# Optimization experiments

Hardware: AMD Instinct MI355X
Metric: run time of the kernel (lower is better)

## Reference

```python
import jax, jax.numpy as jnp
import numpy as np

C, C_H, N_HEAD = 8, 1, 8
B, S, I = 1, 4096, 1024


def setup_inputs() -> dict:
    key = jax.random.key(0)
    ks = jax.random.split(key, 8)
    m = jax.random.normal(ks[0], (B, S, I, C), dtype=jnp.float32)
    mask = jnp.ones((B, S, I), dtype=jnp.float32)
    sc = 0.1
    return {
        "m": m,
        "mask": mask,
        "ln_gamma": jnp.ones((C,), jnp.float32),
        "ln_beta": jnp.zeros((C,), jnp.float32),
        "Wq": jax.random.normal(ks[1], (C, C_H * N_HEAD), jnp.float32) * sc,
        "Wk": jax.random.normal(ks[2], (C, C_H), jnp.float32) * sc,
        "Wv": jax.random.normal(ks[3], (C, C_H), jnp.float32) * sc,
        "Wg": jax.random.normal(ks[4], (C, C_H * N_HEAD), jnp.float32) * sc,
        "bg": jax.random.normal(ks[5], (C_H * N_HEAD,), jnp.float32) * sc,
        "Wo": jax.random.normal(ks[6], (C_H * N_HEAD, C), jnp.float32) * sc,
        "bo": jax.random.normal(ks[7], (C,), jnp.float32) * sc,
    }


def reference(m, mask, ln_gamma, ln_beta, Wq, Wk, Wv, Wg, bg, Wo, bo):
    # m: (B, s, i, c) -> work in (B, i, s, c); mask: (B, s, i) -> (B, i, s)
    mt = jnp.swapaxes(m, -2, -3)
    mk = jnp.swapaxes(mask, -1, -2)
    c_h = Wk.shape[1]
    h = Wq.shape[1] // c_h
    Bz, iz, sz, _ = mt.shape

    # LayerNorm over channel dim (eps=1e-5, population variance)
    mu = jnp.mean(mt, axis=-1, keepdims=True)
    var = jnp.mean(jnp.square(mt - mu), axis=-1, keepdims=True)
    mn = (mt - mu) / jnp.sqrt(var + 1e-5) * ln_gamma + ln_beta  # (B,i,s,c)

    # Masked mean pool over sequences -> global query per residue column
    q = jnp.sum(mn * mk[..., None], axis=-2) / (jnp.sum(mk, axis=-1)[..., None] + 1e-5)  # (B,i,c)

    q = (q @ Wq) * (c_h ** -0.5)          # (B,i,h*c_h)
    k = mn @ Wk                           # (B,i,s,c_h)  shared across heads
    v = mn @ Wv                           # (B,i,s,c_h)
    g = jax.nn.sigmoid(mn @ Wg + bg)      # (B,i,s,h*c_h)

    q = q.reshape(Bz, iz, h, c_h)
    g = g.reshape(Bz, iz, sz, h, c_h)

    bias = 1e9 * (mk - 1.0)               # (B,i,s)
    a = jnp.einsum('bihd,bisd->bihs', q, k) + bias[..., None, :]
    a = jax.nn.softmax(a, axis=-1)        # (B,i,h,s)
    o = jnp.einsum('bihs,bisd->bihd', a, v)  # (B,i,h,c_h)

    o = o[..., None, :, :] * g            # (B,i,s,h,c_h) gated, broadcast over s
    o = o.reshape(Bz, iz, sz, h * c_h) @ Wo + bo  # (B,i,s,c)
    return jnp.swapaxes(o, -2, -3)        # (B,s,i,c)
```

## Files before the change

### kernel.cpp

```cpp
#include <hip/hip_runtime.h>

#define I_LEN 1024

__device__ __forceinline__ float bf2f(unsigned int lo16) {
  unsigned int u = lo16 << 16;
  float f; __builtin_memcpy(&f, &u, 4); return f;
}
__device__ __forceinline__ unsigned int f2bf(float f) {
  unsigned int u; __builtin_memcpy(&u, &f, 4);
  return (u + 0x7FFFu + ((u >> 16) & 1u)) >> 16;
}

__global__ __launch_bounds__(1024) void msa_k1(
    const float* __restrict__ m, const float* __restrict__ mask,
    const float* __restrict__ lng, const float* __restrict__ lnb,
    const float* __restrict__ Wq, const float* __restrict__ Wk,
    const float* __restrict__ Wv, float* __restrict__ o_tab)
{
  __shared__ unsigned int kvs[4096 * 4];
  __shared__ float red[16][4][16];
  __shared__ float fin[4][9];
  __shared__ float qtab[4][8];

  const int t    = threadIdx.x;
  const int col  = t & 3;
  const int r    = t >> 2;
  const int lane = t & 63;
  const int wave = t >> 6;
  const int icol = blockIdx.x * 4 + col;

  float swk = 0.f, swv = 0.f, kb = 0.f, vb = 0.f;
#pragma unroll
  for (int c = 0; c < 8; ++c) {
    swk = fmaf(lng[c], Wk[c], swk);  swv = fmaf(lng[c], Wv[c], swv);
    kb  = fmaf(lnb[c], Wk[c], kb);   vb  = fmaf(lnb[c], Wv[c], vb);
  }

  unsigned int mb = 0;
  float qnx[8] = {0,0,0,0,0,0,0,0};
  float qd = 0.0f;

#pragma unroll 2
  for (int j = 0; j < 16; ++j) {
    const int s = r + 256 * j;
    const float4* mp = (const float4*)(m + (size_t)(s * I_LEN + icol) * 8);
    float4 lo = mp[0], hi = mp[1];
    const float mk = mask[s * I_LEN + icol];
    float x[8] = {lo.x, lo.y, lo.z, lo.w, hi.x, hi.y, hi.z, hi.w};
    float su = 0.f, s2 = 0.f;
#pragma unroll
    for (int c = 0; c < 8; ++c) { su += x[c]; s2 = fmaf(x[c], x[c], s2); }
    const float mu   = su * 0.125f;
    const float var  = s2 * 0.125f - mu * mu;
    const float rstd = rsqrtf(var + 1e-5f);
    float dk = 0.f, dv = 0.f;
#pragma unroll
    for (int c = 0; c < 8; ++c) {
      const float xg = x[c] * lng[c];
      dk = fmaf(xg, Wk[c], dk);
      dv = fmaf(xg, Wv[c], dv);
      x[c] = xg;
    }
    const float kk  = fmaf(rstd, fmaf(-mu, swk, dk), kb);
    const float vv  = fmaf(rstd, fmaf(-mu, swv, dv), vb);
    const float mr  = mk * rstd;
    const float mmr = -mu * mr;
#pragma unroll
    for (int c = 0; c < 8; ++c)
      qnx[c] = fmaf(x[c], mr, fmaf(lng[c], mmr, qnx[c]));
    qd += mk;
    kvs[s * 4 + col] = (f2bf(kk) << 16) | f2bf(vv);
    mb |= (mk > 0.5f ? 1u : 0u) << j;
  }

#pragma unroll
  for (int q = 0; q < 9; ++q) {
    float x = (q < 8) ? qnx[q] : qd;
#pragma unroll
    for (int off = 4; off <= 32; off <<= 1) x += __shfl_xor(x, off, 64);
    if (lane < 4) red[wave][lane][q] = x;
  }
  __syncthreads();
  if (t < 36) {
    int cc = t / 9, q = t - cc * 9;
    float s = 0.f;
#pragma unroll
    for (int w = 0; w < 16; ++w) s += red[w][cc][q];
    fin[cc][q] = s;
  }
  __syncthreads();
  if (t < 32) {
    int cc = t >> 3, h = t & 7;
    const float invd = 1.0f / (fin[cc][8] + 1e-5f);
    float qv = 0.f;
#pragma unroll
    for (int c = 0; c < 8; ++c) {
      const float qn = fmaf(lnb[c], fin[cc][8], fin[cc][c]);
      qv = fmaf(qn * invd, Wq[c * 8 + h], qv);
    }
    qtab[cc][h] = qv;
  }
  __syncthreads();

  float qh[8];
#pragma unroll
  for (int h = 0; h < 8; ++h) qh[h] = qtab[col][h];

  float se[8] = {0,0,0,0,0,0,0,0};
  float sv[8] = {0,0,0,0,0,0,0,0};
#pragma unroll 4
  for (int j = 0; j < 16; ++j) {
    const unsigned int w = kvs[(r + 256 * j) * 4 + col];
    const float kk = bf2f(w >> 16);
    const float vv = bf2f(w & 0xFFFFu);
    const float on = ((mb >> j) & 1u) ? 1.0f : 0.0f;
#pragma unroll
    for (int h = 0; h < 8; ++h) {
      const float e = __expf(qh[h] * kk) * on;
      se[h] += e;
      sv[h] = fmaf(e, vv, sv[h]);
    }
  }
#pragma unroll
  for (int q = 0; q < 16; ++q) {
    float x = (q < 8) ? se[q] : sv[q - 8];
#pragma unroll
    for (int off = 4; off <= 32; off <<= 1) x += __shfl_xor(x, off, 64);
    if (lane < 4) red[wave][lane][q] = x;
  }
  __syncthreads();
  if (t < 32) {
    int cc = t >> 3, h = t & 7;
    float a = 0.f, b = 0.f;
#pragma unroll
    for (int w = 0; w < 16; ++w) { a += red[w][cc][h]; b += red[w][cc][8 + h]; }
    o_tab[(blockIdx.x * 4 + cc) * 8 + h] = b / a;
  }
}

__global__ __launch_bounds__(256, 2) void msa_k2(
    const float* __restrict__ m,
    const float* __restrict__ lng, const float* __restrict__ lnb,
    const float* __restrict__ Wg, const float* __restrict__ bg,
    const float* __restrict__ Wo, const float* __restrict__ bo,
    const float* __restrict__ o_tab, float* __restrict__ out)
{
  const int tid = blockIdx.x * 256 + threadIdx.x;
  const int i = tid & (I_LEN - 1);

  float sgv[8], tbv[8];
#pragma unroll
  for (int h = 0; h < 8; ++h) {
    float s = 0.f, tb = bg[h];
#pragma unroll
    for (int c = 0; c < 8; ++c) {
      s  = fmaf(lng[c], Wg[c * 8 + h], s);
      tb = fmaf(lnb[c], Wg[c * 8 + h], tb);
    }
    sgv[h] = s; tbv[h] = tb;
  }

  const float4* op = (const float4*)(o_tab + i * 8);
  const float4 o1 = op[0], o2 = op[1];
  const float A[8] = {o1.x, o1.y, o1.z, o1.w, o2.x, o2.y, o2.z, o2.w};

#pragma unroll 2
  for (int q = 0; q < 8; ++q) {
    const size_t p = (size_t)tid + (size_t)q * 524288;
    const float4* mp = (const float4*)(m + p * 8);
    const float4 lo = mp[0], hi = mp[1];
    float x[8] = {lo.x, lo.y, lo.z, lo.w, hi.x, hi.y, hi.z, hi.w};
    float su = 0.f, s2 = 0.f;
#pragma unroll
    for (int c = 0; c < 8; ++c) { su += x[c]; s2 = fmaf(x[c], x[c], s2); }
    const float mu   = su * 0.125f;
    const float var  = s2 * 0.125f - mu * mu;
    const float rstd = rsqrtf(var + 1e-5f);
#pragma unroll
    for (int c = 0; c < 8; ++c) x[c] *= lng[c];
    float acc[8];
#pragma unroll
    for (int c = 0; c < 8; ++c) acc[c] = bo[c];
#pragma unroll
    for (int h = 0; h < 8; ++h) {
      float d = 0.f;
#pragma unroll
      for (int c = 0; c < 8; ++c) d = fmaf(x[c], Wg[c * 8 + h], d);
      const float gl = fmaf(rstd, fmaf(-mu, sgv[h], d), tbv[h]);
      const float gv = A[h] / (1.0f + __expf(-gl));
#pragma unroll
      for (int c = 0; c < 8; ++c) acc[c] = fmaf(gv, Wo[h * 8 + c], acc[c]);
    }
    float4* outp = (float4*)(out + p * 8);
    outp[0] = make_float4(acc[0], acc[1], acc[2], acc[3]);
    outp[1] = make_float4(acc[4], acc[5], acc[6], acc[7]);
  }
}

extern "C" void kernel_launch(void* const* d_in, const int* in_sizes, int n_in,
                              void* d_out, int out_size, void* d_ws, size_t ws_size,
                              hipStream_t stream) {
  const float* m    = (const float*)d_in[0];
  const float* mask = (const float*)d_in[1];
  const float* lng  = (const float*)d_in[2];
  const float* lnb  = (const float*)d_in[3];
  const float* Wq   = (const float*)d_in[4];
  const float* Wk   = (const float*)d_in[5];
  const float* Wv   = (const float*)d_in[6];
  const float* Wg   = (const float*)d_in[7];
  const float* bg   = (const float*)d_in[8];
  const float* Wo   = (const float*)d_in[9];
  const float* bo   = (const float*)d_in[10];
  float* out   = (float*)d_out;
  float* o_tab = (float*)d_ws;

  hipLaunchKernelGGL(msa_k1, dim3(256), dim3(1024), 0, stream,
                     m, mask, lng, lnb, Wq, Wk, Wv, o_tab);
  hipLaunchKernelGGL(msa_k2, dim3(2048), dim3(256), 0, stream,
                     m, lng, lnb, Wg, bg, Wo, bo, o_tab, out);
}
```

Baseline: 307.9 us.

## Split attention pass into parallel partial-reduction kernels and precompute quantized gates

Replaces the single low-parallelism column-reduction kernel with four kernels. A 2048-block LayerNorm pass computes K/V (packed as fp16, with a sentinel value for masked rows) and the sigmoid gates, stored as 16-bit fixed point. Small kernels then reduce the per-block partial sums for the pooled query and for the softmax numerator and denominator. The output kernel no longer rereads m or recomputes LayerNorm: it reads the packed gates and writes with nontemporal stores. This trades extra intermediate memory traffic and launches for much higher occupancy, and it lowers gate and K/V precision.

Result: slower. 331.0 us (+7.5%).

```diff
diff --git a/kernel.cpp b/kernel.cpp
--- a/kernel.cpp
+++ b/kernel.cpp
@@ -1,199 +1,312 @@
 #include <hip/hip_runtime.h>
 
 #define I_LEN 1024
-
-__device__ __forceinline__ float bf2f(unsigned int lo16) {
-  unsigned int u = lo16 << 16;
-  float f; __builtin_memcpy(&f, &u, 4); return f;
-}
-__device__ __forceinline__ unsigned int f2bf(float f) {
-  unsigned int u; __builtin_memcpy(&u, &f, 4);
-  return (u + 0x7FFFu + ((u >> 16) & 1u)) >> 16;
-}
-
-__global__ __launch_bounds__(1024) void msa_k1(
+#define S_LEN 4096
+
+typedef float f32x4 __attribute__((ext_vector_type(4)));
+
+__device__ __forceinline__ unsigned int f2h(float f) {
+  _Float16 h = (_Float16)f; unsigned short u;
+  __builtin_memcpy(&u, &h, 2); return (unsigned int)u;
+}
+__device__ __forceinline__ float h2f(unsigned int u) {
+  unsigned short s = (unsigned short)u; _Float16 h;
+  __builtin_memcpy(&h, &s, 2); return (float)h;
+}
+
+__global__ __launch_bounds__(256, 2) void msa_k1a(
     const float* __restrict__ m, const float* __restrict__ mask,
     const float* __restrict__ lng, const float* __restrict__ lnb,
-    const float* __restrict__ Wq, const float* __restrict__ Wk,
-    const float* __restrict__ Wv, float* __restrict__ o_tab)
-{
-  __shared__ unsigned int kvs[4096 * 4];
-  __shared__ float red[16][4][16];
-  __shared__ float fin[4][9];
-  __shared__ float qtab[4][8];
-
-  const int t    = threadIdx.x;
-  const int col  = t & 3;
-  const int r    = t >> 2;
-  const int lane = t & 63;
-  const int wave = t >> 6;
-  const int icol = blockIdx.x * 4 + col;
+    const float* __restrict__ Wk, const float* __restrict__ Wv,
+    const float* __restrict__ Wg, const float* __restrict__ bg,
+    unsigned int* __restrict__ kvS, uint4* __restrict__ glS,
+    float* __restrict__ qpart)
+{
+  const int b  = blockIdx.x;
+  const int cg = b & 15;
+  const int sb = b >> 4;
+  const int t  = threadIdx.x;
+  const int w  = t >> 6;
+  const int l  = t & 63;
+  const int i  = cg * 64 + w * 16 + (l & 15);
+  const int sg = l >> 4;
+  const int s0 = sb * 32 + sg * 8;
 
   float swk = 0.f, swv = 0.f, kb = 0.f, vb = 0.f;
+  float sgv[8], tbv[8];
 #pragma unroll
   for (int c = 0; c < 8; ++c) {
     swk = fmaf(lng[c], Wk[c], swk);  swv = fmaf(lng[c], Wv[c], swv);
     kb  = fmaf(lnb[c], Wk[c], kb);   vb  = fmaf(lnb[c], Wv[c], vb);
   }
-
-  unsigned int mb = 0;
+#pragma unroll
+  for (int h = 0; h < 8; ++h) {
+    float sv_ = 0.f, tb = bg[h];
+#pragma unroll
+    for (int c = 0; c < 8; ++c) {
+      sv_ = fmaf(lng[c], Wg[c * 8 + h], sv_);
+      tb  = fmaf(lnb[c], Wg[c * 8 + h], tb);
+    }
+    sgv[h] = sv_; tbv[h] = tb;
+  }
+
   float qnx[8] = {0,0,0,0,0,0,0,0};
-  float qd = 0.0f;
-
-#pragma unroll 2
-  for (int j = 0; j < 16; ++j) {
-    const int s = r + 256 * j;
-    const float4* mp = (const float4*)(m + (size_t)(s * I_LEN + icol) * 8);
-    float4 lo = mp[0], hi = mp[1];
-    const float mk = mask[s * I_LEN + icol];
-    float x[8] = {lo.x, lo.y, lo.z, lo.w, hi.x, hi.y, hi.z, hi.w};
-    float su = 0.f, s2 = 0.f;
-#pragma unroll
-    for (int c = 0; c < 8; ++c) { su += x[c]; s2 = fmaf(x[c], x[c], s2); }
-    const float mu   = su * 0.125f;
-    const float var  = s2 * 0.125f - mu * mu;
-    const float rstd = rsqrtf(var + 1e-5f);
-    float dk = 0.f, dv = 0.f;
-#pragma unroll
-    for (int c = 0; c < 8; ++c) {
-      const float xg = x[c] * lng[c];
-      dk = fmaf(xg, Wk[c], dk);
-      dv = fmaf(xg, Wv[c], dv);
-      x[c] = xg;
-    }
-    const float kk  = fmaf(rstd, fmaf(-mu, swk, dk), kb);
-    const float vv  = fmaf(rstd, fmaf(-mu, swv, dv), vb);
-    const float mr  = mk * rstd;
-    const float mmr = -mu * mr;
-#pragma unroll
-    for (int c = 0; c < 8; ++c)
-      qnx[c] = fmaf(x[c], mr, fmaf(lng[c], mmr, qnx[c]));
-    qd += mk;
-    kvs[s * 4 + col] = (f2bf(kk) << 16) | f2bf(vv);
-    mb |= (mk > 0.5f ? 1u : 0u) << j;
-  }
-
+  float qd = 0.f;
+
+#pragma unroll
+  for (int half = 0; half < 2; ++half) {
+    float4 L[4], H[4]; float MK[4];
+#pragma unroll
+    for (int r = 0; r < 4; ++r) {
+      const int s = s0 + half * 4 + r;
+      const size_t base = (size_t)(s * I_LEN + i);
+      const float4* mp = (const float4*)(m + base * 8);
+      L[r] = mp[0]; H[r] = mp[1];
+      MK[r] = mask[base];
+    }
+#pragma unroll
+    for (int r = 0; r < 4; ++r) {
+      const int s = s0 + half * 4 + r;
+      const size_t base = (size_t)(s * I_LEN + i);
+      float x[8] = {L[r].x, L[r].y, L[r].z, L[r].w, H[r].x, H[r].y, H[r].z, H[r].w};
+      const float mk = MK[r];
+      float su = 0.f, s2 = 0.f;
+#pragma unroll
+      for (int c = 0; c < 8; ++c) { su += x[c]; s2 = fmaf(x[c], x[c], s2); }
+      const float mu   = su * 0.125f;
+      const float var  = s2 * 0.125f - mu * mu;
+      const float rstd = rsqrtf(var + 1e-5f);
+      float dk = 0.f, dv = 0.f;
+#pragma unroll
+      for (int c = 0; c < 8; ++c) {
+        const float xg = x[c] * lng[c];
+        dk = fmaf(xg, Wk[c], dk);
+        dv = fmaf(xg, Wv[c], dv);
+        x[c] = xg;
+      }
+      const float kk = fmaf(rstd, fmaf(-mu, swk, dk), kb);
+      const float vv = fmaf(rstd, fmaf(-mu, swv, dv), vb);
+
+      unsigned int gw[4];
+#pragma unroll
+      for (int j = 0; j < 4; ++j) {
+        float d0 = 0.f, d1 = 0.f;
+#pragma unroll
+        for (int c = 0; c < 8; ++c) {
+          d0 = fmaf(x[c], Wg[c * 8 + 2 * j],     d0);
+          d1 = fmaf(x[c], Wg[c * 8 + 2 * j + 1], d1);
+        }
+        const float gl0 = fmaf(rstd, fmaf(-mu, sgv[2 * j],     d0), tbv[2 * j]);
+        const float gl1 = fmaf(rstd, fmaf(-mu, sgv[2 * j + 1], d1), tbv[2 * j + 1]);
+        const float g0 = 65535.f / (1.0f + __expf(-gl0));
+        const float g1 = 65535.f / (1.0f + __expf(-gl1));
+        const unsigned int u0 = (unsigned int)__float2int_rn(g0);
+        const unsigned int u1 = (unsigned int)__float2int_rn(g1);
+        gw[j] = u0 | (u1 << 16);
+      }
+      glS[base] = make_uint4(gw[0], gw[1], gw[2], gw[3]);
+      kvS[base] = (mk > 0.5f) ? ((f2h(kk) << 16) | f2h(vv)) : 0xFFFFFFFFu;
+
+      const float mr  = mk * rstd;
+      const float mmr = -mu * mr;
+#pragma unroll
+      for (int c = 0; c < 8; ++c)
+        qnx[c] = fmaf(x[c], mr, fmaf(lng[c], mmr, qnx[c]));
+      qd += mk;
+    }
+  }
+
+  float red[9];
 #pragma unroll
   for (int q = 0; q < 9; ++q) {
     float x = (q < 8) ? qnx[q] : qd;
-#pragma unroll
-    for (int off = 4; off <= 32; off <<= 1) x += __shfl_xor(x, off, 64);
-    if (lane < 4) red[wave][lane][q] = x;
-  }
-  __syncthreads();
-  if (t < 36) {
-    int cc = t / 9, q = t - cc * 9;
-    float s = 0.f;
-#pragma unroll
-    for (int w = 0; w < 16; ++w) s += red[w][cc][q];
-    fin[cc][q] = s;
-  }
-  __syncthreads();
-  if (t < 32) {
-    int cc = t >> 3, h = t & 7;
-    const float invd = 1.0f / (fin[cc][8] + 1e-5f);
-    float qv = 0.f;
-#pragma unroll
-    for (int c = 0; c < 8; ++c) {
-      const float qn = fmaf(lnb[c], fin[cc][8], fin[cc][c]);
-      qv = fmaf(qn * invd, Wq[c * 8 + h], qv);
-    }
-    qtab[cc][h] = qv;
-  }
-  __syncthreads();
-
-  float qh[8];
-#pragma unroll
-  for (int h = 0; h < 8; ++h) qh[h] = qtab[col][h];
+    x += __shfl_xor(x, 16);
+    x += __shfl_xor(x, 32);
+    red[q] = x;
+  }
+  if (l < 16) {
+    float4* pp = (float4*)(qpart + ((size_t)sb * I_LEN + i) * 12);
+    pp[0] = make_float4(red[0], red[1], red[2], red[3]);
+    pp[1] = make_float4(red[4], red[5], red[6], red[7]);
+    pp[2] = make_float4(red[8], 0.f, 0.f, 0.f);
+  }
+}
+
+__global__ __launch_bounds__(64) void msa_k1b(
+    const float* __restrict__ lnb, const float* __restrict__ Wq,
+    const float* __restrict__ qpart, float* __restrict__ qtab)
+{
+  const int l  = threadIdx.x;
+  const int i  = blockIdx.x * 4 + (l & 3);
+  const int sl = l >> 2;
+  float acc[9] = {0,0,0,0,0,0,0,0,0};
+#pragma unroll
+  for (int it = 0; it < 8; ++it) {
+    const int sb = sl + it * 16;
+    const float4* p = (const float4*)(qpart + ((size_t)sb * I_LEN + i) * 12);
+    const float4 a = p[0], b4 = p[1], c4 = p[2];
+    acc[0] += a.x;  acc[1] += a.y;  acc[2] += a.z;  acc[3] += a.w;
+    acc[4] += b4.x; acc[5] += b4.y; acc[6] += b4.z; acc[7] += b4.w;
+    acc[8] += c4.x;
+  }
+#pragma unroll
+  for (int q = 0; q < 9; ++q) {
+    float x = acc[q];
+    x += __shfl_xor(x, 4);
+    x += __shfl_xor(x, 8);
+    x += __shfl_xor(x, 16);
+    x += __shfl_xor(x, 32);
+    acc[q] = x;
+  }
+  if (l < 4) {
+    const float d   = acc[8];
+    const float inv = 1.0f / (d + 1e-5f);
+    float qs[8];
+#pragma unroll
+    for (int c = 0; c < 8; ++c) qs[c] = (acc[c] + lnb[c] * d) * inv;
+    float qv[8];
+#pragma unroll
+    for (int h = 0; h < 8; ++h) {
+      float v = 0.f;
+#pragma unroll
+      for (int c = 0; c < 8; ++c) v = fmaf(qs[c], Wq[c * 8 + h], v);
+      qv[h] = v;
+    }
+    float4* qp = (float4*)(qtab + (size_t)i * 8);
+    qp[0] = make_float4(qv[0], qv[1], qv[2], qv[3]);
+    qp[1] = make_float4(qv[4], qv[5], qv[6], qv[7]);
+  }
+}
+
+__global__ __launch_bounds__(256, 2) void msa_k1c(
+    const unsigned int* __restrict__ kvS, const float* __restrict__ qtab,
+    float* __restrict__ spart)
+{
+  const int b  = blockIdx.x;
+  const int cg = b & 15;
+  const int sb = b >> 4;
+  const int t  = threadIdx.x;
+  const int w  = t >> 6;
+  const int l  = t & 63;
+  const int i  = cg * 64 + w * 16 + (l & 15);
+  const int sg = l >> 4;
+  const int s0 = sb * 32 + sg * 8;
+
+  const float4* qp = (const float4*)(qtab + (size_t)i * 8);
+  const float4 q0 = qp[0], q1 = qp[1];
+  const float qh[8] = {q0.x, q0.y, q0.z, q0.w, q1.x, q1.y, q1.z, q1.w};
 
   float se[8] = {0,0,0,0,0,0,0,0};
   float sv[8] = {0,0,0,0,0,0,0,0};
-#pragma unroll 4
-  for (int j = 0; j < 16; ++j) {
-    const unsigned int w = kvs[(r + 256 * j) * 4 + col];
-    const float kk = bf2f(w >> 16);
-    const float vv = bf2f(w & 0xFFFFu);
-    const float on = ((mb >> j) & 1u) ? 1.0f : 0.0f;
-#pragma unroll
-    for (int h = 0; h < 8; ++h) {
-      const float e = __expf(qh[h] * kk) * on;
-      se[h] += e;
-      sv[h] = fmaf(e, vv, sv[h]);
-    }
-  }
+#pragma unroll
+  for (int half = 0; half < 2; ++half) {
+    unsigned int W[4];
+#pragma unroll
+    for (int r = 0; r < 4; ++r)
+      W[r] = kvS[(size_t)((s0 + half * 4 + r) * I_LEN + i)];
+#pragma unroll
+    for (int r = 0; r < 4; ++r) {
+      const unsigned int wv = W[r];
+      const bool on = (wv != 0xFFFFFFFFu);
+      const float kk = h2f(wv >> 16);
+      const float vv = h2f(wv & 0xFFFFu);
+#pragma unroll
+      for (int h = 0; h < 8; ++h) {
+        const float e = on ? __expf(qh[h] * kk) : 0.0f;
+        se[h] += e;
+        sv[h] = fmaf(e, vv, sv[h]);
+      }
+    }
+  }
+  float red[16];
 #pragma unroll
   for (int q = 0; q < 16; ++q) {
     float x = (q < 8) ? se[q] : sv[q - 8];
-#pragma unroll
-    for (int off = 4; off <= 32; off <<= 1) x += __shfl_xor(x, off, 64);
-    if (lane < 4) red[wave][lane][q] = x;
-  }
-  __syncthreads();
-  if (t < 32) {
-    int cc = t >> 3, h = t & 7;
-    float a = 0.f, b = 0.f;
-#pragma unroll
-    for (int w = 0; w < 16; ++w) { a += red[w][cc][h]; b += red[w][cc][8 + h]; }
-    o_tab[(blockIdx.x * 4 + cc) * 8 + h] = b / a;
+    x += __shfl_xor(x, 16);
+    x += __shfl_xor(x, 32);
+    red[q] = x;
+  }
+  if (l < 16) {
+    float4* pp = (float4*)(spart + ((size_t)sb * I_LEN + i) * 16);
+    pp[0] = make_float4(red[0],  red[1],  red[2],  red[3]);
+    pp[1] = make_float4(red[4],  red[5],  red[6],  red[7]);
+    pp[2] = make_float4(red[8],  red[9],  red[10], red[11]);
+    pp[3] = make_float4(red[12], red[13], red[14], red[15]);
+  }
+}
+
+__global__ __launch_bounds__(64) void msa_k1d(
+    const float* __restrict__ spart, float* __restrict__ o_tab)
+{
+  const int l  = threadIdx.x;
+  const int i  = blockIdx.x * 4 + (l & 3);
+  const int sl = l >> 2;
+  float acc[16] = {0,0,0,0,0,0,0,0,0,0,0,0,0,0,0,0};
+#pragma unroll
+  for (int it = 0; it < 8; ++it) {
+    const int sb = sl + it * 16;
+    const float4* p = (const float4*)(spart + ((size_t)sb * I_LEN + i) * 16);
+    const float4 a = p[0], b4 = p[1], c4 = p[2], d4 = p[3];
+    acc[0]  += a.x;  acc[1]  += a.y;  acc[2]  += a.z;  acc[3]  += a.w;
+    acc[4]  += b4.x; acc[5]  += b4.y; acc[6]  += b4.z; acc[7]  += b4.w;
+    acc[8]  += c4.x; acc[9]  += c4.y; acc[10] += c4.z; acc[11] += c4.w;
+    acc[12] += d4.x; acc[13] += d4.y; acc[14] += d4.z; acc[15] += d4.w;
+  }
+#pragma unroll
+  for (int q = 0; q < 16; ++q) {
+    float x = acc[q];
+    x += __shfl_xor(x, 4);
+    x += __shfl_xor(x, 8);
+    x += __shfl_xor(x, 16);
+    x += __shfl_xor(x, 32);
+    acc[q] = x;
+  }
+  if (l < 4) {
+    float4* op = (float4*)(o_tab + (size_t)i * 8);
+    op[0] = make_float4(acc[8]  / acc[0], acc[9]  / acc[1],
+                        acc[10] / acc[2], acc[11] / acc[3]);
+    op[1] = make_float4(acc[12] / acc[4], acc[13] / acc[5],
+                        acc[14] / acc[6], acc[15] / acc[7]);
   }
 }
 
 __global__ __launch_bounds__(256, 2) void msa_k2(
-    const float* __restrict__ m,
-    const float* __restrict__ lng, const float* __restrict__ lnb,
-    const float* __restrict__ Wg, const float* __restrict__ bg,
+    const uint4* __restrict__ glS, const float* __restrict__ o_tab,
     const float* __restrict__ Wo, const float* __restrict__ bo,
-    const float* __restrict__ o_tab, float* __restrict__ out)
+    float* __restrict__ out)
 {
   const int tid = blockIdx.x * 256 + threadIdx.x;
   const int i = tid & (I_LEN - 1);
 
-  float sgv[8], tbv[8];
-#pragma unroll
-  for (int h = 0; h < 8; ++h) {
-    float s = 0.f, tb = bg[h];
-#pragma unroll
-    for (int c = 0; c < 8; ++c) {
-      s  = fmaf(lng[c], Wg[c * 8 + h], s);
-      tb = fmaf(lnb[c], Wg[c * 8 + h], tb);
-    }
-    sgv[h] = s; tbv[h] = tb;
-  }
-
-  const float4* op = (const float4*)(o_tab + i * 8);
+  const float4* op = (const float4*)(o_tab + (size_t)i * 8);
   const float4 o1 = op[0], o2 = op[1];
-  const float A[8] = {o1.x, o1.y, o1.z, o1.w, o2.x, o2.y, o2.z, o2.w};
+  const float kfx = 1.0f / 65535.f;
+  const float A[8] = {o1.x * kfx, o1.y * kfx, o1.z * kfx, o1.w * kfx,
+                      o2.x * kfx, o2.y * kfx, o2.z * kfx, o2.w * kfx};
 
 #pragma unroll 2
   for (int q = 0; q < 8; ++q) {
     const size_t p = (size_t)tid + (size_t)q * 524288;
-    const float4* mp = (const float4*)(m + p * 8);
-    const float4 lo = mp[0], hi = mp[1];
-    float x[8] = {lo.x, lo.y, lo.z, lo.w, hi.x, hi.y, hi.z, hi.w};
-    float su = 0.f, s2 = 0.f;
-#pragma unroll
-    for (int c = 0; c < 8; ++c) { su += x[c]; s2 = fmaf(x[c], x[c], s2); }
-    const float mu   = su * 0.125f;
-    const float var  = s2 * 0.125f - mu * mu;
-    const float rstd = rsqrtf(var + 1e-5f);
-#pragma unroll
-    for (int c = 0; c < 8; ++c) x[c] *= lng[c];
+    const uint4 G = glS[p];
+    const unsigned int gw[4] = {G.x, G.y, G.z, G.w};
     float acc[8];
 #pragma unroll
     for (int c = 0; c < 8; ++c) acc[c] = bo[c];
 #pragma unroll
-    for (int h = 0; h < 8; ++h) {
-      float d = 0.f;
-#pragma unroll
-      for (int c = 0; c < 8; ++c) d = fmaf(x[c], Wg[c * 8 + h], d);
-      const float gl = fmaf(rstd, fmaf(-mu, sgv[h], d), tbv[h]);
-      const float gv = A[h] / (1.0f + __expf(-gl));
-#pragma unroll
-      for (int c = 0; c < 8; ++c) acc[c] = fmaf(gv, Wo[h * 8 + c], acc[c]);
-    }
-    float4* outp = (float4*)(out + p * 8);
-    outp[0] = make_float4(acc[0], acc[1], acc[2], acc[3]);
-    outp[1] = make_float4(acc[4], acc[5], acc[6], acc[7]);
+    for (int j = 0; j < 4; ++j) {
+      const float gv0 = A[2 * j]     * (float)(gw[j] & 0xFFFFu);
+      const float gv1 = A[2 * j + 1] * (float)(gw[j] >> 16);
+#pragma unroll
+      for (int c = 0; c < 8; ++c) {
+        acc[c] = fmaf(gv0, Wo[(2 * j) * 8 + c], acc[c]);
+        acc[c] = fmaf(gv1, Wo[(2 * j + 1) * 8 + c], acc[c]);
+      }
+    }
+    f32x4* outp = (f32x4*)(out + p * 8);
+    f32x4 r0 = {acc[0], acc[1], acc[2], acc[3]};
+    f32x4 r1 = {acc[4], acc[5], acc[6], acc[7]};
+    __builtin_nontemporal_store(r0, outp);
+    __builtin_nontemporal_store(r1, outp + 1);
   }
 }
 
@@ -211,11 +324,24 @@
   const float* bg   = (const float*)d_in[8];
   const float* Wo   = (const float*)d_in[9];
   const float* bo   = (const float*)d_in[10];
-  float* out   = (float*)d_out;
-  float* o_tab = (float*)d_ws;
-
-  hipLaunchKernelGGL(msa_k1, dim3(256), dim3(1024), 0, stream,
-                     m, mask, lng, lnb, Wq, Wk, Wv, o_tab);
+  float* out = (float*)d_out;
+
+  char* ws = (char*)d_ws;
+  float*        o_tab = (float*)ws;
+  float*        qtab  = (float*)(ws + ((size_t)64 << 10));
+  unsigned int* kvS   = (unsigned int*)(ws + ((size_t)1 << 20));
+  uint4*        glS   = (uint4*)(ws + ((size_t)32 << 20));
+  float*        qpart = (float*)(ws + ((size_t)104 << 20));
+  float*        spart = (float*)(ws + ((size_t)112 << 20));
+
+  hipLaunchKernelGGL(msa_k1a, dim3(2048), dim3(256), 0, stream,
+                     m, mask, lng, lnb, Wk, Wv, Wg, bg, kvS, glS, qpart);
+  hipLaunchKernelGGL(msa_k1b, dim3(256), dim3(64), 0, stream,
+                     lnb, Wq, qpart, qtab);
+  hipLaunchKernelGGL(msa_k1c, dim3(2048), dim3(256), 0, stream,
+                     kvS, qtab, spart);
+  hipLaunchKernelGGL(msa_k1d, dim3(256), dim3(64), 0, stream,
+                     spart, o_tab);
   hipLaunchKernelGGL(msa_k2, dim3(2048), dim3(256), 0, stream,
-                     m, lng, lnb, Wg, bg, Wo, bo, o_tab, out);
-}
+                     glS, o_tab, Wo, bo, out);
+}
```
